# Optimization experiments

Hardware: AMD Instinct MI355X
Metric: run time of the kernel (lower is better)

## Reference

```python
import jax, jax.numpy as jnp
import numpy as np


def setup_inputs() -> dict:
    key = jax.random.key(0)
    ks = jax.random.split(key, 32)
    B, S, H, E, Vs, T = 32, 400, 512, 300, 200, 32
    EN, V = 50000, 50200
    rn = lambda k, shape, s=0.05: jax.random.normal(k, shape, jnp.float32) * s
    return {
        'encoder_hidden': rn(ks[0], (B, S, 2 * H), 1.0),
        'hidden0': rn(ks[1], (B, H), 1.0),
        'user_embed': rn(ks[2], (B, E), 1.0),
        'W_embed': rn(ks[3], (EN, E), 1.0),
        'W_ih': rn(ks[4], (3 * H, E)), 'W_hh': rn(ks[5], (3 * H, H)),
        'b_ih': rn(ks[6], (3 * H,)), 'b_hh': rn(ks[7], (3 * H,)),
        'Wk_c': rn(ks[8], (2 * H, H)), 'bk_c': rn(ks[9], (H,)),
        'Wq_c': rn(ks[10], (H, H)), 'bq_c': rn(ks[11], (H,)),
        'we_c': rn(ks[12], (H,)), 'be_c': rn(ks[13], (1,)),
        'Wk_u': rn(ks[14], (E, H)), 'bk_u': rn(ks[15], (H,)),
        'Wq_u': rn(ks[16], (H, H)), 'bq_u': rn(ks[17], (H,)),
        'we_u': rn(ks[18], (H,)), 'be_u': rn(ks[19], (1,)),
        'Wc': rn(ks[20], (3 * H + 2 * E, H)),
        'Wg': rn(ks[21], (3 * H + E,)), 'bg': rn(ks[22], (1,)),
        'Wgen': rn(ks[23], (H, EN)),
        'src_mask': jnp.ones((B, S), jnp.int32),
        'tgt_': jax.random.randint(ks[24], (B, T), 0, EN),
        'specific_vocab': jax.random.randint(ks[25], (B, Vs), 0, EN),
        'vocab_size': V,
    }


def reference(encoder_hidden, hidden0, user_embed, W_embed, W_ih, W_hh, b_ih, b_hh,
              Wk_c, bk_c, Wq_c, bq_c, we_c, be_c, Wk_u, bk_u, Wq_u, bq_u, we_u, be_u,
              Wc, Wg, bg, Wgen, src_mask, tgt_, specific_vocab, vocab_size):
    B, T = tgt_.shape
    # teacher forcing: prev token embed, step 0 uses <s> token id 1
    tgt_embed = W_embed[tgt_]                                  # [B,T,E]
    init_embed = jnp.broadcast_to(W_embed[1], (B, 1, W_embed.shape[1]))
    prev = jnp.concatenate([init_embed, tgt_embed[:, :T - 1]], axis=1)
    xs = jnp.swapaxes(prev, 0, 1)                              # [T,B,E]

    user_vocab_emb = W_embed[specific_vocab]                   # [B,Vs,E]
    proj_key_c = encoder_hidden @ Wk_c + bk_c                  # [B,S,H]
    proj_key_u = user_vocab_emb @ Wk_u + bk_u                  # [B,Vs,H]
    mask = src_mask != 0
    batch_idx = jnp.arange(B)[:, None]

    def gru_cell(h, x):
        gi = x @ W_ih.T + b_ih
        gh = h @ W_hh.T + b_hh
        i_r, i_z, i_n = jnp.split(gi, 3, axis=-1)
        h_r, h_z, h_n = jnp.split(gh, 3, axis=-1)
        r = jax.nn.sigmoid(i_r + h_r)
        z = jax.nn.sigmoid(i_z + h_z)
        n = jnp.tanh(i_n + r * h_n)
        return (1.0 - z) * n + z * h

    def step(h, x):
        h = gru_cell(h, x)                                     # [B,H]
        q = h
        # Bahdanau attention over encoder states
        sc = jnp.tanh((q @ Wq_c + bq_c)[:, None, :] + proj_key_c) @ we_c + be_c  # [B,S]
        sc = jnp.where(mask, sc, -1e9)
        ac = jax.nn.softmax(sc, axis=-1)
        ctx_c = jnp.einsum('bs,bsd->bd', ac, encoder_hidden)   # [B,2H]
        # Bahdanau attention over user-specific vocab embeddings
        su = jnp.tanh((q @ Wq_u + bq_u)[:, None, :] + proj_key_u) @ we_u + be_u  # [B,Vs]
        au = jax.nn.softmax(su, axis=-1)
        ctx_u = jnp.einsum('bv,bve->be', au, user_vocab_emb)   # [B,E]
        ch = jnp.tanh(jnp.concatenate([q, ctx_c, ctx_u, user_embed], axis=-1) @ Wc)
        gen_prob = jax.nn.softmax(ch @ Wgen, axis=-1)          # [B,embed_num]
        gen_prob = jnp.pad(gen_prob, ((0, 0), (0, vocab_size - gen_prob.shape[-1])))
        copy_prob = jnp.zeros((B, vocab_size), gen_prob.dtype).at[batch_idx, specific_vocab].add(au)
        copy_p = jax.nn.sigmoid(jnp.concatenate([ctx_c, q, ctx_u], axis=-1) @ Wg + bg[0])[:, None]
        mix = copy_p * copy_prob + (1.0 - copy_p) * gen_prob   # [B,vocab]
        return h, mix

    _, probs = jax.lax.scan(step, hidden0, xs)                 # [T,B,V]
    return jnp.swapaxes(probs, 0, 1)                           # [B,T,V]
```

## Files before the change

kernel.cpp:

```cpp
#include <hip/hip_runtime.h>


typedef __attribute__((ext_vector_type(8))) short short8;
typedef __attribute__((ext_vector_type(4))) float f32x4;
typedef unsigned short us;

#define SCW (-2.8853900817779268f)

__device__ __forceinline__ float bf2f(us u) {
  return __uint_as_float(((unsigned)u) << 16);
}
__device__ __forceinline__ us f2bf(float f) {
  unsigned x = __float_as_uint(f);
  unsigned r = x + 0x7fffu + ((x >> 16) & 1u);
  return (us)(r >> 16);
}
__device__ __forceinline__ float fsigmoid(float x) { return 1.f / (1.f + __expf(-x)); }
__device__ __forceinline__ float ftanh(float x) {
  float t = __expf(-2.f * fabsf(x));
  float r = (1.f - t) / (1.f + t);
  return x >= 0.f ? r : -r;
}
__device__ __forceinline__ float ftanh_fast(float x) {
  float u = exp2f(SCW * fabsf(x));
  float r = (1.f - u) * __builtin_amdgcn_rcpf(1.f + u);
  return copysignf(r, x);
}
__device__ __forceinline__ void unpack8(uint4 v, float* f) {
  f[0] = bf2f((us)(v.x & 0xffff)); f[1] = bf2f((us)(v.x >> 16));
  f[2] = bf2f((us)(v.y & 0xffff)); f[3] = bf2f((us)(v.y >> 16));
  f[4] = bf2f((us)(v.z & 0xffff)); f[5] = bf2f((us)(v.z >> 16));
  f[6] = bf2f((us)(v.w & 0xffff)); f[7] = bf2f((us)(v.w >> 16));
}

struct PP {
  const float *enc, *hidden0, *Wk_c, *Wk_u, *Wq_c, *Wq_u, *Wc, *W_ih, *W_hh, *W_embed;
  const int *tgt, *sv;
  us *encb, *hball, *WkcT, *WkuT, *WqcuT, *WcT, *WihT, *WhhF, *xe, *uve;
};

__device__ void tcast_job(const float* __restrict__ src, us* __restrict__ dst,
                          int R, int C, int Rpad, int x, int y, float scale,
                          int lt, float* tb) {
  int tx = lt & 31, ty = lt >> 5;
  int c0 = x * 32, r0 = y * 32;
#pragma unroll
  for (int i = 0; i < 4; ++i) {
    int r = r0 + ty + i * 8, c = c0 + tx;
    tb[(ty + i * 8) * 33 + tx] = (r < R && c < C) ? src[(size_t)r * C + c] : 0.f;
  }
  __syncthreads();
#pragma unroll
  for (int i = 0; i < 4; ++i) {
    int c = c0 + ty + i * 8, rr = r0 + tx;
    if (c < C && rr < Rpad)
      dst[(size_t)c * Rpad + rr] = f2bf(scale * tb[tx * 33 + ty + i * 8]);
  }
}

__global__ __launch_bounds__(256) void k_prep(PP P) {
  __shared__ float tb[32 * 33];
  const int bid = blockIdx.x, tid = threadIdx.x;
  if (bid < 1024) {
    for (int i = bid * 256 + tid; i < 3276800; i += 1024 * 256) {
      float4 v = ((const float4*)P.enc)[i];
      ushort4 o;
      o.x = f2bf(v.x); o.y = f2bf(v.y); o.z = f2bf(v.z); o.w = f2bf(v.w);
      ((ushort4*)P.encb)[i] = o;
    }
  } else if (bid < 1040) {
    int i = (bid - 1024) * 256 + tid;
    float4 v = ((const float4*)P.hidden0)[i];
    ushort4 o;
    o.x = f2bf(v.x); o.y = f2bf(v.y); o.z = f2bf(v.z); o.w = f2bf(v.w);
    ((ushort4*)P.hball)[i] = o;
  } else if (bid < 1552) {
    int j = bid - 1040;
    tcast_job(P.Wk_c, P.WkcT, 1024, 512, 1024, j & 15, j >> 4, SCW, tid, tb);
  } else if (bid < 1712) {
    int j = bid - 1552;
    tcast_job(P.Wk_u, P.WkuT, 300, 512, 320, j % 16, j / 16, SCW, tid, tb);
  } else if (bid < 1968) {
    int j = bid - 1712;
    tcast_job(P.Wq_c, P.WqcuT, 512, 512, 512, j & 15, j >> 4, SCW, tid, tb);
  } else if (bid < 2224) {
    int j = bid - 1968;
    tcast_job(P.Wq_u, P.WqcuT + 512ull * 512, 512, 512, 512, j & 15, j >> 4, SCW, tid, tb);
  } else if (bid < 3296) {
    int j = bid - 2224;
    tcast_job(P.Wc, P.WcT, 2136, 512, 2144, j % 16, j / 16, 1.f, tid, tb);
  } else if (bid < 3680) {
    int row = (bid - 3296) * 4 + (tid >> 6), k = tid & 63;
    for (int kk = k; kk < 320; kk += 64)
      P.WihT[(size_t)row * 320 + kk] =
          (kk < 300) ? f2bf(P.W_ih[(size_t)row * 300 + kk]) : (us)0;
  } else if (bid < 4064) {
    int job = (bid - 3680) * 4 + (tid >> 6), l = tid & 63;
    int q = job / 192, rem = job - q * 192, lt2 = rem >> 4, kt = rem & 15;
    int localrow = lt2 * 16 + (l & 15);
    int g = localrow >> 6, jj = localrow & 63;
    const float* src =
        P.W_hh + (size_t)(g * 512 + q * 64 + jj) * 512 + kt * 32 + (l >> 4) * 8;
    us* dst = P.WhhF + (((size_t)(q * 12 + lt2) * 16 + kt) * 64 + l) * 8;
#pragma unroll
    for (int i = 0; i < 8; ++i) dst[i] = f2bf(src[i]);
  } else if (bid < 4320) {
    int r = (bid - 4064) * 4 + (tid >> 6), k = tid & 63;
    int t = r >> 5, b = r & 31;
    int tok = (t == 0) ? 1 : P.tgt[b * 32 + (t - 1)];
    const float* src = P.W_embed + (size_t)tok * 300;
    for (int kk = k; kk < 320; kk += 64)
      P.xe[(size_t)r * 320 + kk] = (kk < 300) ? f2bf(src[kk]) : (us)0;
  } else {
    int row = (bid - 4320) * 4 + (tid >> 6), k = tid & 63;
    int tok = P.sv[row];
    const float* src = P.W_embed + (size_t)tok * 300;
    for (int kk = k; kk < 320; kk += 64)
      P.uve[(size_t)row * 320 + kk] = (kk < 300) ? f2bf(src[kk]) : (us)0;
  }
}

__global__ __launch_bounds__(256) void k_tcastX(const float* __restrict__ src0,
                                                us* __restrict__ dst0,
                                                int R, int C, int Rpad,
                                                size_t srcB, size_t dstB) {
  __shared__ float tile[32 * 33];
  const float* src = src0 + (size_t)blockIdx.z * srcB;
  us* dst = dst0 + (size_t)blockIdx.z * dstB;
  tcast_job(src, dst, R, C, Rpad, blockIdx.x, blockIdx.y, 1.f, threadIdx.x, tile);
}
__global__ __launch_bounds__(256) void k_tcastXb(const us* __restrict__ src0,
                                                 us* __restrict__ dst0,
                                                 int R, int C, int Rpad,
                                                 size_t srcB, size_t dstB) {
  __shared__ us tile[32][33];
  const us* src = src0 + (size_t)blockIdx.z * srcB;
  us* dst = dst0 + (size_t)blockIdx.z * dstB;
  int c0 = blockIdx.x * 32, r0 = blockIdx.y * 32;
  int tx = threadIdx.x & 31, ty = threadIdx.x >> 5;
#pragma unroll
  for (int i = 0; i < 4; ++i) {
    int r = r0 + ty + i * 8, c = c0 + tx;
    tile[ty + i * 8][tx] = (r < R && c < C) ? src[(size_t)r * C + c] : (us)0;
  }
  __syncthreads();
#pragma unroll
  for (int i = 0; i < 4; ++i) {
    int c = c0 + ty + i * 8, rr = r0 + tx;
    if (c < C && rr < Rpad) dst[(size_t)c * Rpad + rr] = tile[tx][ty + i * 8];
  }
}

template <int MODE, bool NM = false>
__global__ __launch_bounds__(512) void gemm_bt(const us* __restrict__ A,
                                               const us* __restrict__ BT,
                                               int M, int N, int K, int Ntiles,
                                               const float* __restrict__ bias,
                                               float bscale,
                                               us* __restrict__ outB,
                                               float* __restrict__ outF,
                                               float* __restrict__ rowsum) {
  __shared__ us sh[12288];
  __shared__ float rs[256];
  us* As = sh;
  us* Bs = sh + 8192;
  const int tid = threadIdx.x;
  const int lane = tid & 63, wid = tid >> 6;
  const int wr = wid >> 1, wc = wid & 1;
  const int bx = blockIdx.x;
  int mt, nt;
  if (NM) { mt = bx & 3; nt = bx >> 2; }
  else { mt = bx / Ntiles; nt = bx - mt * Ntiles; }
  const int m0 = mt * 256, n0 = nt * 128;
  f32x4 acc[4][4] = {};
  for (int kk = 0; kk < K; kk += 32) {
    uint4 av0, av1, bv;
    {
      int c = tid, row = c >> 2, c8 = (c & 3) * 8;
      av0 = *(const uint4*)(A + (size_t)(m0 + row) * K + kk + c8);
      c = tid + 512; row = c >> 2; c8 = (c & 3) * 8;
      av1 = *(const uint4*)(A + (size_t)(m0 + row) * K + kk + c8);
      c = tid; row = c >> 2; c8 = (c & 3) * 8;
      int nr = n0 + row; if (nr > N - 1) nr = N - 1;
      bv = *(const uint4*)(BT + (size_t)nr * K + kk + c8);
    }
    __syncthreads();
    ((uint4*)As)[tid] = av0;
    ((uint4*)As)[tid + 512] = av1;
    ((uint4*)Bs)[tid] = bv;
    __syncthreads();
    short8 af[4], bfr[4];
#pragma unroll
    for (int m = 0; m < 4; ++m)
      af[m] = *(const short8*)(As + (wr * 64 + m * 16 + (lane & 15)) * 32 + (lane >> 4) * 8);
#pragma unroll
    for (int n = 0; n < 4; ++n)
      bfr[n] = *(const short8*)(Bs + (wc * 64 + n * 16 + (lane & 15)) * 32 + (lane >> 4) * 8);
#pragma unroll
    for (int m = 0; m < 4; ++m)
#pragma unroll
      for (int n = 0; n < 4; ++n)
        acc[m][n] = __builtin_amdgcn_mfma_f32_16x16x32_bf16(af[m], bfr[n], acc[m][n], 0, 0, 0);
  }
  if (MODE == 0) {
#pragma unroll
    for (int m = 0; m < 4; ++m)
#pragma unroll
      for (int n = 0; n < 4; ++n)
#pragma unroll
        for (int reg = 0; reg < 4; ++reg) {
          int r = m0 + wr * 64 + m * 16 + (lane >> 4) * 4 + reg;
          int c = n0 + wc * 64 + n * 16 + (lane & 15);
          outB[(size_t)r * N + c] = f2bf(acc[m][n][reg] + bscale * bias[c]);
        }
  } else {
    if (tid < 256) rs[tid] = 0.f;
    __syncthreads();
#pragma unroll
    for (int m = 0; m < 4; ++m) {
#pragma unroll
      for (int reg = 0; reg < 4; ++reg) {
        int rloc = wr * 64 + m * 16 + (lane >> 4) * 4 + reg;
        float s = 0.f;
#pragma unroll
        for (int n = 0; n < 4; ++n) {
          int c = n0 + wc * 64 + n * 16 + (lane & 15);
          float e = (c < N) ? __expf(acc[m][n][reg]) : 0.f;
          if (c < N) {
            int r = m0 + rloc;
            size_t obase = (size_t)((r & 31) * 32 + (r >> 5)) * 50200;
            outF[obase + c] = e;
          }
          s += e;
        }
        s += __shfl_xor(s, 1, 64); s += __shfl_xor(s, 2, 64);
        s += __shfl_xor(s, 4, 64); s += __shfl_xor(s, 8, 64);
        if ((lane & 15) == 0) atomicAdd(&rs[rloc], s);
      }
    }
    __syncthreads();
    if (tid < 256) atomicAdd(&rowsum[m0 + tid], rs[tid]);
  }
}

__global__ __launch_bounds__(1024, 1) void gemm_v(const us* __restrict__ A,
                                                  const us* __restrict__ BT,
                                                  us* __restrict__ outB,
                                                  float* __restrict__ rowsum) {
  __shared__ us shp[16384];
  __shared__ float rs[256];
  us* As = shp;
  us* Bs = shp + 8192;
  const int tid = threadIdx.x;
  const int lane = tid & 63, wid = tid >> 6;
  const int wr2 = wid >> 2, wc2 = wid & 3;
  const int bx = blockIdx.x;
  const int mt = bx & 3, nt = bx >> 2;
  const int m0 = mt * 256, n0 = nt * 256;
  const int N = 50000;
  const int srow = tid >> 2, sc8 = (tid & 3) * 8;
  int bnr = n0 + srow; if (bnr > N - 1) bnr = N - 1;
  f32x4 acc[4][4] = {};
  for (int kk = 0; kk < 512; kk += 32) {
    uint4 av = *(const uint4*)(A + (size_t)(m0 + srow) * 512 + kk + sc8);
    uint4 bv = *(const uint4*)(BT + (size_t)bnr * 512 + kk + sc8);
    __syncthreads();
    ((uint4*)As)[tid] = av;
    ((uint4*)Bs)[tid] = bv;
    __syncthreads();
    short8 af[4], bfr[4];
#pragma unroll
    for (int m = 0; m < 4; ++m)
      af[m] = *(const short8*)(As + (wr2 * 64 + m * 16 + (lane & 15)) * 32 + (lane >> 4) * 8);
#pragma unroll
    for (int n = 0; n < 4; ++n)
      bfr[n] = *(const short8*)(Bs + (wc2 * 64 + n * 16 + (lane & 15)) * 32 + (lane >> 4) * 8);
#pragma unroll
    for (int m = 0; m < 4; ++m)
#pragma unroll
      for (int n = 0; n < 4; ++n)
        acc[m][n] = __builtin_amdgcn_mfma_f32_16x16x32_bf16(af[m], bfr[n], acc[m][n], 0, 0, 0);
  }
  if (tid < 256) rs[tid] = 0.f;
  __syncthreads();
  for (int g = 0; g < 4; ++g) {
    if (wr2 == g) {
#pragma unroll
      for (int m = 0; m < 4; ++m)
#pragma unroll
        for (int reg = 0; reg < 4; ++reg) {
          int rloc_g = m * 16 + (lane >> 4) * 4 + reg;
          float s = 0.f;
#pragma unroll
          for (int n = 0; n < 4; ++n) {
            int c = n0 + wc2 * 64 + n * 16 + (lane & 15);
            float e = (c < N) ? __expf(acc[m][n][reg]) : 0.f;
            shp[rloc_g * 256 + wc2 * 64 + n * 16 + (lane & 15)] = f2bf(e);
            s += e;
          }
          s += __shfl_xor(s, 1, 64); s += __shfl_xor(s, 2, 64);
          s += __shfl_xor(s, 4, 64); s += __shfl_xor(s, 8, 64);
          if ((lane & 15) == 0) atomicAdd(&rs[g * 64 + rloc_g], s);
        }
    }
    __syncthreads();
#pragma unroll
    for (int k2 = 0; k2 < 2; ++k2) {
      int idx = tid + k2 * 1024;
      int l = idx >> 5, u = idx & 31;
      int r = m0 + g * 64 + l;
      size_t obase = (size_t)((r & 31) * 32 + (r >> 5)) * 50200;
      *(uint4*)(outB + obase + n0 + u * 8) = *(const uint4*)(shp + l * 256 + u * 8);
    }
    __syncthreads();
  }
  if (tid < 256) atomicAdd(&rowsum[m0 + tid], rs[tid]);
}

template <int MODE>
__global__ __launch_bounds__(256) void gemm_med(const us* __restrict__ A,
                                                const us* __restrict__ BT,
                                                int M, int N, int K, int Ntiles,
                                                const float* __restrict__ bias,
                                                float bscale,
                                                us* __restrict__ outB) {
  __shared__ us As[64 * 32];
  __shared__ us Bs[128 * 32];
  const int tid = threadIdx.x, lane = tid & 63, w = tid >> 6;
  const int bx = blockIdx.x;
  const int mt = bx / Ntiles, nt = bx - mt * Ntiles;
  const int m0 = mt * 64, n0 = nt * 128;
  f32x4 acc[4][2] = {};
  for (int kk = 0; kk < K; kk += 32) {
    uint4 av, bv0, bv1;
    av = *(const uint4*)(A + (size_t)(m0 + (tid >> 2)) * K + kk + (tid & 3) * 8);
    {
      int i0 = tid * 2, i1 = tid * 2 + 1;
      bv0 = *(const uint4*)(BT + (size_t)(n0 + (i0 >> 2)) * K + kk + (i0 & 3) * 8);
      bv1 = *(const uint4*)(BT + (size_t)(n0 + (i1 >> 2)) * K + kk + (i1 & 3) * 8);
    }
    __syncthreads();
    ((uint4*)As)[tid] = av;
    ((uint4*)Bs)[tid * 2] = bv0;
    ((uint4*)Bs)[tid * 2 + 1] = bv1;
    __syncthreads();
    short8 af[4], bf0, bf1;
#pragma unroll
    for (int m = 0; m < 4; ++m)
      af[m] = *(const short8*)(As + (m * 16 + (lane & 15)) * 32 + (lane >> 4) * 8);
    bf0 = *(const short8*)(Bs + ((w * 2 + 0) * 16 + (lane & 15)) * 32 + (lane >> 4) * 8);
    bf1 = *(const short8*)(Bs + ((w * 2 + 1) * 16 + (lane & 15)) * 32 + (lane >> 4) * 8);
#pragma unroll
    for (int m = 0; m < 4; ++m) {
      acc[m][0] = __builtin_amdgcn_mfma_f32_16x16x32_bf16(af[m], bf0, acc[m][0], 0, 0, 0);
      acc[m][1] = __builtin_amdgcn_mfma_f32_16x16x32_bf16(af[m], bf1, acc[m][1], 0, 0, 0);
    }
  }
#pragma unroll
  for (int m = 0; m < 4; ++m)
#pragma unroll
    for (int q = 0; q < 2; ++q)
#pragma unroll
      for (int reg = 0; reg < 4; ++reg) {
        int r = m0 + m * 16 + (lane >> 4) * 4 + reg;
        int c = n0 + (w * 2 + q) * 16 + (lane & 15);
        float v = acc[m][q][reg];
        if (MODE == 0) v += bscale * bias[c];
        else v = ftanh_fast(v);
        outB[(size_t)r * N + c] = f2bf(v);
      }
}

struct FP {
  const us* frag; const us* gib; const float* bhh; const float* hidden0;
  us* hball; int* arrive;
  const us* encb; const us* WkcT; const float* bkc; us* pkc;
  const us* uve; const us* WkuT; const float* bku; us* pku;
  const float* Wgen; us* WT;
  const float* enc; us* encTp;
  us* uveTp;
};

__device__ void gru_body(const FP& P, int q, int tid, char* pool) {
  us* hs = (us*)pool;
  float* gh = (float*)(pool + 32768);
  const int lane = tid & 63, w = tid >> 6;
  short8 bfr[16];
  {
    const us* fb = P.frag + (((size_t)(q * 12 + w) * 16) * 64 + lane) * 8;
#pragma unroll
    for (int kt = 0; kt < 16; ++kt) bfr[kt] = *(const short8*)(fb + (size_t)kt * 512);
  }
  float hprev[3], bh0[3], bh1[3], bh2[3];
#pragma unroll
  for (int s = 0; s < 3; ++s) {
    int i = tid + s * 768;
    if (i < 2048) {
      int b = i >> 6, jj = i & 63, j = q * 64 + jj;
      hprev[s] = P.hidden0[b * 512 + j];
      bh0[s] = P.bhh[j]; bh1[s] = P.bhh[512 + j]; bh2[s] = P.bhh[1024 + j];
    }
  }
  const int sw = (lane & 7) << 3;
  for (int t = 0; t < 32; ++t) {
    float gi0[3], gi1[3], gi2[3];
#pragma unroll
    for (int s = 0; s < 3; ++s) {
      int i = tid + s * 768;
      if (i < 2048) {
        int b = i >> 6, jj = i & 63, j = q * 64 + jj;
        size_t gbase = (size_t)(t * 32 + b) * 1536;
        gi0[s] = bf2f(P.gib[gbase + j]);
        gi1[s] = bf2f(P.gib[gbase + 512 + j]);
        gi2[s] = bf2f(P.gib[gbase + 1024 + j]);
      }
    }
    if (t > 0) {
      if (tid == 0) {
        while (__hip_atomic_load(P.arrive + (t - 1), __ATOMIC_ACQUIRE,
                                 __HIP_MEMORY_SCOPE_AGENT) < 8) {
          __builtin_amdgcn_s_sleep(1);
        }
      }
      __syncthreads();
    }
    const us* hp = P.hball + (size_t)t * 16384;
    for (int i = tid; i < 2048; i += 768)
      ((uint4*)hs)[i ^ ((i >> 6) & 7)] = *(const uint4*)(hp + i * 8);
    __syncthreads();
    f32x4 acc0 = {}, acc1 = {};
#pragma unroll
    for (int kt = 0; kt < 16; ++kt) {
      int base0 = ((lane & 15) * 512 + kt * 32 + (lane >> 4) * 8) ^ sw;
      int base1 = (((lane & 15) + 16) * 512 + kt * 32 + (lane >> 4) * 8) ^ sw;
      short8 a0 = *(const short8*)(hs + base0);
      short8 a1 = *(const short8*)(hs + base1);
      acc0 = __builtin_amdgcn_mfma_f32_16x16x32_bf16(a0, bfr[kt], acc0, 0, 0, 0);
      acc1 = __builtin_amdgcn_mfma_f32_16x16x32_bf16(a1, bfr[kt], acc1, 0, 0, 0);
    }
    {
      int col = w * 16 + (lane & 15);
#pragma unroll
      for (int reg = 0; reg < 4; ++reg) {
        gh[col * 33 + ((lane >> 4) * 4 + reg)] = acc0[reg];
        gh[col * 33 + (16 + (lane >> 4) * 4 + reg)] = acc1[reg];
      }
    }
    __syncthreads();
    us* hbn = P.hball + (size_t)(t + 1) * 16384;
#pragma unroll
    for (int s = 0; s < 3; ++s) {
      int i = tid + s * 768;
      if (i < 2048) {
        int b = i >> 6, jj = i & 63, j = q * 64 + jj;
        float g0 = gh[jj * 33 + b] + bh0[s];
        float g1 = gh[(64 + jj) * 33 + b] + bh1[s];
        float g2 = gh[(128 + jj) * 33 + b] + bh2[s];
        float r_ = fsigmoid(gi0[s] + g0);
        float z_ = fsigmoid(gi1[s] + g1);
        float n_ = ftanh(gi2[s] + r_ * g2);
        float hv = (1.f - z_) * n_ + z_ * hprev[s];
        hprev[s] = hv;
        hbn[b * 512 + j] = f2bf(hv);
      }
    }
    __syncthreads();
    if (tid == 0)
      __hip_atomic_fetch_add(P.arrive + t, 1, __ATOMIC_RELEASE,
                             __HIP_MEMORY_SCOPE_AGENT);
  }
}

__device__ void gemm0_body(const us* A, const us* BT, int N, int K,
                           int mt, int nt, const float* bias, float bscale,
                           us* outB, int tid, char* pool) {
  us* As = (us*)pool;
  us* Bs = (us*)(pool + 16384);
  const bool act = tid < 512;
  const int lane = tid & 63, wid = (tid >> 6) & 7;
  const int wr = wid >> 1, wc = wid & 1;
  const int m0 = mt * 256, n0 = nt * 128;
  f32x4 acc[4][4] = {};
  for (int kk = 0; kk < K; kk += 32) {
    uint4 av0 = {0, 0, 0, 0}, av1 = {0, 0, 0, 0}, bv = {0, 0, 0, 0};
    if (act) {
      int c = tid, row = c >> 2, c8 = (c & 3) * 8;
      av0 = *(const uint4*)(A + (size_t)(m0 + row) * K + kk + c8);
      av1 = *(const uint4*)(A + (size_t)(m0 + 128 + row) * K + kk + c8);
      int nr = n0 + row; if (nr > N - 1) nr = N - 1;
      bv = *(const uint4*)(BT + (size_t)nr * K + kk + c8);
    }
    __syncthreads();
    if (act) {
      ((uint4*)As)[tid] = av0;
      ((uint4*)As)[tid + 512] = av1;
      ((uint4*)Bs)[tid] = bv;
    }
    __syncthreads();
    if (act) {
      short8 af[4], bfr[4];
#pragma unroll
      for (int m = 0; m < 4; ++m)
        af[m] = *(const short8*)(As + (wr * 64 + m * 16 + (lane & 15)) * 32 + (lane >> 4) * 8);
#pragma unroll
      for (int n = 0; n < 4; ++n)
        bfr[n] = *(const short8*)(Bs + (wc * 64 + n * 16 + (lane & 15)) * 32 + (lane >> 4) * 8);
#pragma unroll
      for (int m = 0; m < 4; ++m)
#pragma unroll
        for (int n = 0; n < 4; ++n)
          acc[m][n] = __builtin_amdgcn_mfma_f32_16x16x32_bf16(af[m], bfr[n], acc[m][n], 0, 0, 0);
    }
  }
  if (act) {
#pragma unroll
    for (int m = 0; m < 4; ++m)
#pragma unroll
      for (int n = 0; n < 4; ++n)
#pragma unroll
        for (int reg = 0; reg < 4; ++reg) {
          int r = m0 + wr * 64 + m * 16 + (lane >> 4) * 4 + reg;
          int c = n0 + wc * 64 + n * 16 + (lane & 15);
          outB[(size_t)r * N + c] = f2bf(acc[m][n][reg] + bscale * bias[c]);
        }
  }
}

__global__ __launch_bounds__(768, 1) void k_fat(FP P) {
  __shared__ char pool[58368];
  const int bid = blockIdx.x, tid = threadIdx.x;
  if (bid < 8) { gru_body(P, bid, tid, pool); return; }
  if (bid < 208) {
    int j = bid - 8;
    gemm0_body(P.encb, P.WkcT, 512, 1024, j >> 2, j & 3, P.bkc, SCW, P.pkc, tid, pool);
    return;
  }
  if (bid < 308) {
    int j = bid - 208;
    gemm0_body(P.uve, P.WkuT, 512, 320, j >> 2, j & 3, P.bku, SCW, P.pku, tid, pool);
    return;
  }
  const int g = tid >> 8, lt = tid & 255;
  const int tx = lt & 31, ty = lt >> 5;
  float* tb = (float*)(pool + g * 4224);
  if (bid < 830) {
    int base = (bid - 308) * 3 + g;
    for (int it = 0; it < 16; ++it) {
      int sub = base + it * 1566;
      bool valid = sub < 25008;
      int x = valid ? sub % 1563 : 0, y = valid ? sub / 1563 : 0;
      int c0 = x * 32, r0 = y * 32;
      if (valid) {
#pragma unroll
        for (int i = 0; i < 4; ++i) {
          int r = r0 + ty + i * 8, c = c0 + tx;
          tb[(ty + i * 8) * 33 + tx] =
              (c < 50000) ? P.Wgen[(size_t)r * 50000 + c] : 0.f;
        }
      }
      __syncthreads();
      if (valid) {
#pragma unroll
        for (int i = 0; i < 4; ++i) {
          int c = c0 + ty + i * 8;
          if (c < 50000)
            P.WT[(size_t)c * 512 + r0 + tx] = f2bf(tb[tx * 33 + ty + i * 8]);
        }
      }
      __syncthreads();
    }
    return;
  }
  if (bid < 1108) {
    int base = (bid - 830) * 3 + g;
    for (int it = 0; it < 16; ++it) {
      int sub = base + it * 834;
      bool valid = sub < 13312;
      int x = sub & 31, rem = sub >> 5;
      int y = rem % 13, z = rem / 13;
      const float* src = P.enc + (size_t)z * 409600;
      us* dst = P.encTp + (size_t)z * 425984;
      int c0 = x * 32, r0 = y * 32;
      if (valid) {
#pragma unroll
        for (int i = 0; i < 4; ++i) {
          int r = r0 + ty + i * 8, c = c0 + tx;
          tb[(ty + i * 8) * 33 + tx] = (r < 400) ? src[(size_t)r * 1024 + c] : 0.f;
        }
      }
      __syncthreads();
      if (valid) {
#pragma unroll
        for (int i = 0; i < 4; ++i) {
          int c = c0 + ty + i * 8, rr = r0 + tx;
          if (rr < 416) dst[(size_t)c * 416 + rr] = f2bf(tb[tx * 33 + ty + i * 8]);
        }
      }
      __syncthreads();
    }
    return;
  }
  {
    us* tbu = (us*)tb;
    int base = (bid - 1108) * 3 + g;
    for (int it = 0; it < 16; ++it) {
      int sub = base + it * 141;
      bool valid = sub < 2240;
      int x = sub % 10, rem = sub / 10;
      int y = rem % 7, z = rem / 7;
      const us* src = P.uve + (size_t)z * 64000;
      us* dst = P.uveTp + (size_t)z * 71680;
      int c0 = x * 32, r0 = y * 32;
      if (valid) {
#pragma unroll
        for (int i = 0; i < 4; ++i) {
          int r = r0 + ty + i * 8, c = c0 + tx;
          tbu[(ty + i * 8) * 33 + tx] = (r < 200) ? src[(size_t)r * 320 + c] : (us)0;
        }
      }
      __syncthreads();
      if (valid) {
#pragma unroll
        for (int i = 0; i < 4; ++i) {
          int c = c0 + ty + i * 8, rr = r0 + tx;
          if (rr < 224) dst[(size_t)c * 224 + rr] = tbu[tx * 33 + ty + i * 8];
        }
      }
      __syncthreads();
    }
  }
}

__global__ __launch_bounds__(256) void k_scores(const us* __restrict__ Qall,
                                                const us* __restrict__ pkc,
                                                const us* __restrict__ pku,
                                                const float* __restrict__ wec,
                                                const float* __restrict__ bec,
                                                const float* __restrict__ weu,
                                                const float* __restrict__ beu,
                                                const int* __restrict__ src_mask,
                                                float* __restrict__ sc_enc,
                                                float* __restrict__ sc_usr) {
  __shared__ us q[16 * 512];
  const int bid = blockIdx.x;
  const bool enc = bid < 1600;
  int b, s0, th, qoff, S;
  if (enc) {
    b = bid / 50;
    int r = bid % 50;
    s0 = (r >> 1) * 16; th = r & 1; qoff = 0; S = 400;
  } else {
    int j = bid - 1600;
    b = j / 26;
    int r = j % 26;
    s0 = (r >> 1) * 16; th = r & 1; qoff = 512; S = 200;
  }
  for (int i = threadIdx.x; i < 1024; i += 256) {
    int tt = th * 16 + (i >> 6), c8 = (i & 63) * 8;
    ((uint4*)q)[i] = *(const uint4*)(Qall + (size_t)(tt * 32 + b) * 1024 + qoff + c8);
  }
  const int w = threadIdx.x >> 6, lane = threadIdx.x & 63;
  const int d0 = lane * 8;
  const float* we = enc ? wec : weu;
  float wef[8];
  {
    float4 w0 = *(const float4*)(we + d0);
    float4 w1 = *(const float4*)(we + d0 + 4);
    wef[0] = w0.x; wef[1] = w0.y; wef[2] = w0.z; wef[3] = w0.w;
    wef[4] = w1.x; wef[5] = w1.y; wef[6] = w1.z; wef[7] = w1.w;
  }
  const float bias = enc ? bec[0] : beu[0];
  float pkf[4][8];
  int ss[4], validv[4], maskedv[4];
#pragma unroll
  for (int si = 0; si < 4; ++si) {
    int s = s0 + w * 4 + si;
    validv[si] = (s < S);
    int sc = validv[si] ? s : (S - 1);
    ss[si] = sc;
    const us* pk = enc ? pkc + ((size_t)b * 400 + sc) * 512
                       : pku + ((size_t)b * 200 + sc) * 512;
    unpack8(*(const uint4*)(pk + d0), pkf[si]);
    maskedv[si] = enc ? (src_mask[b * 400 + sc] == 0) : 0;
  }
  __syncthreads();
  for (int tl = 0; tl < 16; ++tl) {
    short8 qv = *(const short8*)(q + tl * 512 + d0);
    float qf[8];
#pragma unroll
    for (int d = 0; d < 8; ++d) qf[d] = bf2f((us)qv[d]);
#pragma unroll
    for (int si = 0; si < 4; ++si) {
      float a = 0.f;
#pragma unroll
      for (int d = 0; d < 8; ++d) {
        float x = qf[d] + pkf[si][d];
        float u = exp2f(-fabsf(x));
        float r2v = (1.f - u) * __builtin_amdgcn_rcpf(1.f + u);
        a = fmaf(copysignf(r2v, -x), wef[d], a);
      }
#pragma unroll
      for (int m = 1; m < 64; m <<= 1) a += __shfl_xor(a, m, 64);
      if (lane == 0 && validv[si]) {
        int t = th * 16 + tl;
        float v = a + bias;
        if (enc) sc_enc[(size_t)(t * 32 + b) * 400 + ss[si]] = maskedv[si] ? -1e9f : v;
        else sc_usr[(size_t)(t * 32 + b) * 200 + ss[si]] = v;
      }
    }
  }
}

__device__ __forceinline__ float bmax256(float v, float* r4, int tid) {
#pragma unroll
  for (int m = 1; m < 64; m <<= 1) v = fmaxf(v, __shfl_xor(v, m, 64));
  if ((tid & 63) == 0) r4[tid >> 6] = v;
  __syncthreads();
  float x = fmaxf(fmaxf(r4[0], r4[1]), fmaxf(r4[2], r4[3]));
  __syncthreads();
  return x;
}
__device__ __forceinline__ float bsum256(float v, float* r4, int tid) {
#pragma unroll
  for (int m = 1; m < 64; m <<= 1) v += __shfl_xor(v, m, 64);
  if ((tid & 63) == 0) r4[tid >> 6] = v;
  __syncthreads();
  float x = r4[0] + r4[1] + r4[2] + r4[3];
  __syncthreads();
  return x;
}

__global__ __launch_bounds__(256) void k_soft2(const float* __restrict__ sc_enc,
                                               const float* __restrict__ sc_usr,
                                               us* __restrict__ AC,
                                               us* __restrict__ AU,
                                               float* __restrict__ aual,
                                               float* __restrict__ cp_acc,
                                               const us* __restrict__ hball,
                                               const float* __restrict__ ue,
                                               const float* __restrict__ Wg,
                                               us* __restrict__ catall) {
  __shared__ float r4[4];
  int bid = blockIdx.x, tid = threadIdx.x;
  if (bid < 1024) {
    int t = bid >> 5, b = bid & 31;
    float v0 = (tid < 400) ? sc_enc[(size_t)bid * 400 + tid] : -3e38f;
    float v1 = (tid + 256 < 400) ? sc_enc[(size_t)bid * 400 + tid + 256] : -3e38f;
    float mx = bmax256(fmaxf(v0, v1), r4, tid);
    float e0 = (tid < 400) ? __expf(v0 - mx) : 0.f;
    float e1 = (tid + 256 < 400) ? __expf(v1 - mx) : 0.f;
    float inv = 1.f / bsum256(e0 + e1, r4, tid);
    us* ACb = AC + (size_t)(b * 32 + t) * 416;
    if (tid < 400) ACb[tid] = f2bf(e0 * inv);
    int s2 = tid + 256;
    if (s2 < 400) ACb[s2] = f2bf(e1 * inv);
    else if (s2 < 416) ACb[s2] = 0;
  } else if (bid < 2048) {
    int rr = bid - 1024;
    int t = rr >> 5, b = rr & 31;
    float v0 = (tid < 200) ? sc_usr[(size_t)rr * 200 + tid] : -3e38f;
    float mx = bmax256(v0, r4, tid);
    float e0 = (tid < 200) ? __expf(v0 - mx) : 0.f;
    float inv = 1.f / bsum256(e0, r4, tid);
    us* AUb = AU + (size_t)(b * 32 + t) * 224;
    if (tid < 200) {
      float a = e0 * inv;
      AUb[tid] = f2bf(a);
      aual[(size_t)rr * 200 + tid] = a;
    } else if (tid < 224) {
      AUb[tid] = 0;
    }
  } else if (bid < 2304) {
    int w = tid >> 6, lane = tid & 63;
    int row = (bid - 2048) * 4 + w;
    int t = row >> 5, b = row & 31;
    us* rowp = catall + (size_t)row * 2144;
    const us* hb = hball + (size_t)(t + 1) * 16384 + b * 512;
    *(uint4*)(rowp + lane * 8) = *(const uint4*)(hb + lane * 8);
    for (int i = lane; i < 308; i += 64)
      rowp[1836 + i] = (i < 300) ? f2bf(ue[b * 300 + i]) : (us)0;
  } else {
    int w = tid >> 6, lane = tid & 63, d0 = lane * 8;
#pragma unroll
    for (int k = 0; k < 2; ++k) {
      int row = (bid - 2304) * 8 + w * 2 + k;
      int t = row >> 5, b = row & 31;
      float hv[8];
      unpack8(*(const uint4*)(hball + (size_t)(t + 1) * 16384 + b * 512 + d0), hv);
      float4 g0 = *(const float4*)(Wg + 1024 + d0);
      float4 g1 = *(const float4*)(Wg + 1024 + d0 + 4);
      float a = hv[0] * g0.x + hv[1] * g0.y + hv[2] * g0.z + hv[3] * g0.w +
                hv[4] * g1.x + hv[5] * g1.y + hv[6] * g1.z + hv[7] * g1.w;
#pragma unroll
      for (int m = 1; m < 64; m <<= 1) a += __shfl_xor(a, m, 64);
      if (lane == 0) atomicAdd(&cp_acc[row], a);
    }
  }
}

__device__ void ctx_core(const us* Ab, const us* Bb, const float* Wg,
                         us* catall, float* cp_acc, int b, int N, int Kp,
                         int n0, int catOff, int wgOff, int Nvalid, int tid,
                         us* As, us* Bs, float* gaccs) {
  const int lane = tid & 63, w = tid >> 6;
  if (tid < 32) gaccs[tid] = 0.f;
  f32x4 acc[2][2] = {};
  for (int kk = 0; kk < Kp; kk += 32) {
    uint4 av, bv0, bv1;
    if (tid < 128) av = *(const uint4*)(Ab + (size_t)(tid >> 2) * Kp + kk + (tid & 3) * 8);
    {
      int i0 = tid * 2, row0 = i0 >> 2, c0 = (i0 & 3) * 8;
      int i1 = tid * 2 + 1, row1 = i1 >> 2, c1 = (i1 & 3) * 8;
      int nr0 = n0 + row0; if (nr0 > N - 1) nr0 = N - 1;
      int nr1 = n0 + row1; if (nr1 > N - 1) nr1 = N - 1;
      bv0 = *(const uint4*)(Bb + (size_t)nr0 * Kp + kk + c0);
      bv1 = *(const uint4*)(Bb + (size_t)nr1 * Kp + kk + c1);
    }
    __syncthreads();
    if (tid < 128) ((uint4*)As)[tid] = av;
    ((uint4*)Bs)[tid * 2] = bv0;
    ((uint4*)Bs)[tid * 2 + 1] = bv1;
    __syncthreads();
    short8 a0 = *(const short8*)(As + ((lane & 15)) * 32 + (lane >> 4) * 8);
    short8 a1 = *(const short8*)(As + (16 + (lane & 15)) * 32 + (lane >> 4) * 8);
#pragma unroll
    for (int qq = 0; qq < 2; ++qq) {
      short8 bf_ = *(const short8*)(Bs + ((w * 2 + qq) * 16 + (lane & 15)) * 32 + (lane >> 4) * 8);
      acc[0][qq] = __builtin_amdgcn_mfma_f32_16x16x32_bf16(a0, bf_, acc[0][qq], 0, 0, 0);
      acc[1][qq] = __builtin_amdgcn_mfma_f32_16x16x32_bf16(a1, bf_, acc[1][qq], 0, 0, 0);
    }
  }
#pragma unroll
  for (int mt = 0; mt < 2; ++mt)
#pragma unroll
    for (int qq = 0; qq < 2; ++qq)
#pragma unroll
      for (int reg = 0; reg < 4; ++reg) {
        int t_ = mt * 16 + (lane >> 4) * 4 + reg;
        int c = n0 + (w * 2 + qq) * 16 + (lane & 15);
        if (c < Nvalid) {
          float v = acc[mt][qq][reg];
          catall[(size_t)(t_ * 32 + b) * 2144 + catOff + c] = f2bf(v);
          atomicAdd(&gaccs[t_], v * Wg[wgOff + c]);
        }
      }
  __syncthreads();
  if (tid < 32) atomicAdd(&cp_acc[tid * 32 + b], gaccs[tid]);
}

__global__ __launch_bounds__(256) void k_ctx2(const us* __restrict__ AC,
                                              const us* __restrict__ encTp,
                                              const us* __restrict__ AU,
                                              const us* __restrict__ uveTp,
                                              const float* __restrict__ Wg,
                                              us* __restrict__ catall,
                                              float* __restrict__ cp_acc) {
  __shared__ us As[32 * 32];
  __shared__ us Bs[128 * 32];
  __shared__ float gaccs[32];
  int bid = blockIdx.x, tid = threadIdx.x;
  if (bid < 256) {
    int b = bid >> 3, nt = bid & 7;
    ctx_core(AC + (size_t)b * 32 * 416, encTp + (size_t)b * 1024 * 416, Wg,
             catall, cp_acc, b, 1024, 416, nt * 128, 512, 0, 1024, tid, As, Bs, gaccs);
  } else {
    int j = bid - 256;
    int b = j / 3, nt = j % 3;
    ctx_core(AU + (size_t)b * 32 * 224, uveTp + (size_t)b * 320 * 224, Wg,
             catall, cp_acc, b, 320, 224, nt * 128, 1536, 1536, 300, tid, As, Bs, gaccs);
  }
}

__global__ __launch_bounds__(256) void k_finalize(float* __restrict__ out,
                                                  const float* __restrict__ rowsum,
                                                  const float* __restrict__ cp_acc,
                                                  const float* __restrict__ bg,
                                                  const float* __restrict__ au_all,
                                                  const int* __restrict__ sv) {
  int r = blockIdx.x, t = threadIdx.x;
  int b = r & 31, tt = r >> 5;
  float cp = fsigmoid(cp_acc[r] + bg[0]);
  float scale = (1.f - cp) / rowsum[r];
  float* base = out + (size_t)(b * 32 + tt) * 50200;
  float4* b4 = (float4*)base;
  for (int i = t; i < 12550; i += 256) {
    if (i < 12500) {
      float4 v = b4[i];
      v.x *= scale; v.y *= scale; v.z *= scale; v.w *= scale;
      b4[i] = v;
    } else {
      b4[i] = make_float4(0.f, 0.f, 0.f, 0.f);
    }
  }
  __syncthreads();
  if (t < 200) {
    int idx = sv[b * 200 + t];
    atomicAdd(base + idx, cp * au_all[(size_t)r * 200 + t]);
  }
}

__global__ __launch_bounds__(256) void k_finalize2(const us* __restrict__ expb,
                                                   const float* __restrict__ rowsum,
                                                   const float* __restrict__ cp_acc,
                                                   const float* __restrict__ bg,
                                                   const float* __restrict__ au_all,
                                                   const int* __restrict__ sv,
                                                   float* __restrict__ out) {
  int r = blockIdx.x, t = threadIdx.x;
  int b = r & 31, tt = r >> 5;
  float cp = fsigmoid(cp_acc[r] + bg[0]);
  float scale = (1.f - cp) / rowsum[r];
  size_t obase = (size_t)(b * 32 + tt) * 50200;
  const uint4* eb = (const uint4*)(expb + obase);
  float4* ob = (float4*)(out + obase);
  for (int i = t; i < 6275; i += 256) {
    float4 o0, o1;
    if (i < 6250) {
      uint4 ev = eb[i];
      o0.x = bf2f((us)(ev.x & 0xffff)) * scale; o0.y = bf2f((us)(ev.x >> 16)) * scale;
      o0.z = bf2f((us)(ev.y & 0xffff)) * scale; o0.w = bf2f((us)(ev.y >> 16)) * scale;
      o1.x = bf2f((us)(ev.z & 0xffff)) * scale; o1.y = bf2f((us)(ev.z >> 16)) * scale;
      o1.z = bf2f((us)(ev.w & 0xffff)) * scale; o1.w = bf2f((us)(ev.w >> 16)) * scale;
    } else {
      o0 = make_float4(0.f, 0.f, 0.f, 0.f);
      o1 = o0;
    }
    ob[i * 2] = o0;
    ob[i * 2 + 1] = o1;
  }
  __syncthreads();
  if (t < 200) {
    int idx = sv[b * 200 + t];
    atomicAdd(out + obase + idx, cp * au_all[(size_t)r * 200 + t]);
  }
}


extern "C" void kernel_launch(void* const* d_in, const int* in_sizes, int n_in,
                              void* d_out, int out_size, void* d_ws, size_t ws_size,
                              hipStream_t stream) {
  (void)in_sizes; (void)n_in; (void)out_size;
  const float* enc = (const float*)d_in[0];
  const float* hidden0 = (const float*)d_in[1];
  const float* user_embed = (const float*)d_in[2];
  const float* W_embed = (const float*)d_in[3];
  const float* W_ih = (const float*)d_in[4];
  const float* W_hh = (const float*)d_in[5];
  const float* b_ih = (const float*)d_in[6];
  const float* b_hh = (const float*)d_in[7];
  const float* Wk_c = (const float*)d_in[8];
  const float* bk_c = (const float*)d_in[9];
  const float* Wq_c = (const float*)d_in[10];
  const float* bq_c = (const float*)d_in[11];
  const float* we_c = (const float*)d_in[12];
  const float* be_c = (const float*)d_in[13];
  const float* Wk_u = (const float*)d_in[14];
  const float* bk_u = (const float*)d_in[15];
  const float* Wq_u = (const float*)d_in[16];
  const float* bq_u = (const float*)d_in[17];
  const float* we_u = (const float*)d_in[18];
  const float* be_u = (const float*)d_in[19];
  const float* Wc = (const float*)d_in[20];
  const float* Wg = (const float*)d_in[21];
  const float* bg = (const float*)d_in[22];
  const float* Wgen = (const float*)d_in[23];
  const int* src_mask = (const int*)d_in[24];
  const int* tgt = (const int*)d_in[25];
  const int* sv = (const int*)d_in[26];
  float* out = (float*)d_out;

  char* base = (char*)d_ws;
  size_t off = 0;
  auto take = [&](size_t bytes) {
    char* p = base + off;
    off += (bytes + 255) & ~(size_t)255;
    return p;
  };
  us* WT = (us*)take(50000ull * 512 * 2);
  char* R0 = take(32ull * 1024 * 416 * 2);
  us* encb = (us*)R0;
  char* RCD = take(12800ull * 512 * 2 + 6400ull * 512 * 2);
  us* pkc = (us*)RCD;
  us* pku = (us*)(RCD + 12800ull * 512 * 2);
  us* AC = (us*)RCD;
  us* AU = (us*)(RCD + 860160);
  float* aual = (float*)(RCD + 860160 + 458752);
  us* catall = (us*)(RCD + 860160 + 458752 + 819200);
  us* chb = (us*)(RCD + 860160 + 458752 + 819200 + 4390912);
  us* uve = (us*)take(6400ull * 320 * 2);
  us* uveTp = (us*)take(32ull * 320 * 224 * 2);
  char* RG = take(2700000);
  us* WkcT = (us*)RG;
  us* WihT = (us*)(RG + 1048576);
  us* xe = (us*)(RG + 1048576 + 983040);
  us* WkuT = (us*)take(512ull * 320 * 2);
  us* WqcuT = (us*)take(1024ull * 512 * 2);
  us* WcT = (us*)take(512ull * 2144 * 2);
  us* WhhF = (us*)take(1536ull * 512 * 2);
  us* gib = (us*)take(1024ull * 1536 * 2);
  us* hball = (us*)take(33ull * 16384 * 2);
  us* Qall = (us*)take(1024ull * 1024 * 2);
  float* sc_enc = (float*)take(1024ull * 400 * 4);
  float* sc_usr = (float*)take(1024ull * 200 * 4);
  float* bqcu = (float*)take(1024 * 4);
  float* cp_acc = (float*)take(1024 * 4);
  float* rsum = (float*)take(1024 * 4);
  int* arrive = (int*)take(32 * 4);
  size_t expb_bytes = 1024ull * 50200 * 2;
  bool big_ws = (ws_size >= off + expb_bytes + 256);
  us* expb = big_ws ? (us*)take(expb_bytes) : nullptr;
  us* encTp = big_ws ? expb : (us*)R0;

  hipMemcpyAsync(bqcu, bq_c, 512 * 4, hipMemcpyDeviceToDevice, stream);
  hipMemcpyAsync(bqcu + 512, bq_u, 512 * 4, hipMemcpyDeviceToDevice, stream);
  hipMemsetAsync(rsum, 0, 1024 * 4, stream);
  hipMemsetAsync(cp_acc, 0, 1024 * 4, stream);
  hipMemsetAsync(arrive, 0, 32 * 4, stream);

  PP pp;
  pp.enc = enc; pp.hidden0 = hidden0; pp.Wk_c = Wk_c; pp.Wk_u = Wk_u;
  pp.Wq_c = Wq_c; pp.Wq_u = Wq_u; pp.Wc = Wc; pp.W_ih = W_ih; pp.W_hh = W_hh;
  pp.W_embed = W_embed; pp.tgt = tgt; pp.sv = sv;
  pp.encb = encb; pp.hball = hball; pp.WkcT = WkcT; pp.WkuT = WkuT;
  pp.WqcuT = WqcuT; pp.WcT = WcT; pp.WihT = WihT; pp.WhhF = WhhF;
  pp.xe = xe; pp.uve = uve;
  k_prep<<<5920, 256, 0, stream>>>(pp);
  gemm_med<0><<<192, 256, 0, stream>>>(xe, WihT, 1024, 1536, 320, 12, b_ih, 1.f, gib);

  FP fp;
  fp.frag = WhhF; fp.gib = gib; fp.bhh = b_hh; fp.hidden0 = hidden0;
  fp.hball = hball; fp.arrive = arrive;
  fp.encb = encb; fp.WkcT = WkcT; fp.bkc = bk_c; fp.pkc = pkc;
  fp.uve = uve; fp.WkuT = WkuT; fp.bku = bk_u; fp.pku = pku;
  fp.Wgen = Wgen; fp.WT = WT; fp.enc = enc; fp.encTp = encTp; fp.uveTp = uveTp;

  if (big_ws) {
    k_fat<<<1155, 768, 0, stream>>>(fp);
  } else {
    k_tcastX<<<dim3(1563, 16, 1), 256, 0, stream>>>(Wgen, WT, 512, 50000, 512, 0, 0);
    gemm_bt<0><<<200, 512, 0, stream>>>(encb, WkcT, 12800, 512, 1024, 4, bk_c, SCW,
                                        pkc, nullptr, nullptr);
    gemm_bt<0><<<100, 512, 0, stream>>>(uve, WkuT, 6400, 512, 320, 4, bk_u, SCW,
                                        pku, nullptr, nullptr);
    k_tcastX<<<dim3(32, 13, 32), 256, 0, stream>>>(enc, encTp, 400, 1024, 416,
                                                   400ull * 1024, 1024ull * 416);
    k_tcastXb<<<dim3(10, 7, 32), 256, 0, stream>>>(uve, uveTp, 200, 320, 224,
                                                   200ull * 320, 320ull * 224);
    k_fat<<<8, 768, 0, stream>>>(fp);
  }

  gemm_med<0><<<128, 256, 0, stream>>>(hball + 16384, WqcuT, 1024, 1024, 512, 8,
                                       bqcu, SCW, Qall);
  k_scores<<<2432, 256, 0, stream>>>(Qall, pkc, pku, we_c, be_c, we_u, be_u,
                                     src_mask, sc_enc, sc_usr);
  k_soft2<<<2432, 256, 0, stream>>>(sc_enc, sc_usr, AC, AU, aual, cp_acc,
                                    hball, user_embed, Wg, catall);
  k_ctx2<<<352, 256, 0, stream>>>(AC, encTp, AU, uveTp, Wg, catall, cp_acc);
  gemm_med<2><<<64, 256, 0, stream>>>(catall, WcT, 1024, 512, 2144, 4, nullptr,
                                      1.f, chb);
  if (big_ws) {
    gemm_v<<<784, 1024, 0, stream>>>(chb, WT, expb, rsum);
    k_finalize2<<<1024, 256, 0, stream>>>(expb, rsum, cp_acc, bg, aual, sv, out);
  } else {
    gemm_bt<1, true><<<4 * 391, 512, 0, stream>>>(chb, WT, 1024, 50000, 512, 391,
                                                  nullptr, 1.f, nullptr, out, rsum);
    k_finalize<<<1024, 256, 0, stream>>>(out, rsum, cp_acc, bg, aual, sv);
  }
}
```

Baseline: 705.3 us.

## Retile vocab GEMM to 256x128 blocks with swizzled LDS and per-block flags

The large vocabulary-projection GEMM moves from 1024-thread 256x256 tiles to 512-thread 256x128 tiles with launch bounds allowing several blocks per CU. It uses a K-step of 64, XOR-swizzled shared-memory layouts to reduce bank conflicts, and a per-m-subtile epilogue that stages rows through padded LDS. The goal is better occupancy and latency hiding in the dominant GEMM, at the cost of loading A twice as often per output column. Separately, the GRU step barrier replaces a shared atomic counter with per-block flag stores that each waiter polls, avoiding contention on one atomic.

Result: slower. 841.8 us (+19.4%).

```diff
diff --git a/kernel.cpp b/kernel.cpp
--- a/kernel.cpp
+++ b/kernel.cpp
@@ -243,74 +243,102 @@
   }
 }
 
-__global__ __launch_bounds__(1024, 1) void gemm_v(const us* __restrict__ A,
+__global__ __launch_bounds__(512, 4) void gemm_v2(const us* __restrict__ A,
                                                   const us* __restrict__ BT,
                                                   us* __restrict__ outB,
                                                   float* __restrict__ rowsum) {
-  __shared__ us shp[16384];
+  __shared__ us sh[24576];
   __shared__ float rs[256];
-  us* As = shp;
-  us* Bs = shp + 8192;
+  us* As = sh;
+  us* Bs = sh + 16384;
   const int tid = threadIdx.x;
   const int lane = tid & 63, wid = tid >> 6;
-  const int wr2 = wid >> 2, wc2 = wid & 3;
+  const int wr = wid >> 1, wc = wid & 1;
   const int bx = blockIdx.x;
   const int mt = bx & 3, nt = bx >> 2;
-  const int m0 = mt * 256, n0 = nt * 256;
+  const int m0 = mt * 256, n0 = nt * 128;
   const int N = 50000;
-  const int srow = tid >> 2, sc8 = (tid & 3) * 8;
-  int bnr = n0 + srow; if (bnr > N - 1) bnr = N - 1;
   f32x4 acc[4][4] = {};
-  for (int kk = 0; kk < 512; kk += 32) {
-    uint4 av = *(const uint4*)(A + (size_t)(m0 + srow) * 512 + kk + sc8);
-    uint4 bv = *(const uint4*)(BT + (size_t)bnr * 512 + kk + sc8);
-    __syncthreads();
-    ((uint4*)As)[tid] = av;
-    ((uint4*)Bs)[tid] = bv;
-    __syncthreads();
-    short8 af[4], bfr[4];
-#pragma unroll
-    for (int m = 0; m < 4; ++m)
-      af[m] = *(const short8*)(As + (wr2 * 64 + m * 16 + (lane & 15)) * 32 + (lane >> 4) * 8);
-#pragma unroll
-    for (int n = 0; n < 4; ++n)
-      bfr[n] = *(const short8*)(Bs + (wc2 * 64 + n * 16 + (lane & 15)) * 32 + (lane >> 4) * 8);
-#pragma unroll
-    for (int m = 0; m < 4; ++m)
-#pragma unroll
-      for (int n = 0; n < 4; ++n)
-        acc[m][n] = __builtin_amdgcn_mfma_f32_16x16x32_bf16(af[m], bfr[n], acc[m][n], 0, 0, 0);
+  for (int kk = 0; kk < 512; kk += 64) {
+    uint4 av[4], bv[2];
+#pragma unroll
+    for (int k = 0; k < 4; ++k) {
+      int idx = tid + k * 512;
+      int row = idx >> 3, c8 = (idx & 7) * 8;
+      av[k] = *(const uint4*)(A + (size_t)(m0 + row) * 512 + kk + c8);
+    }
+#pragma unroll
+    for (int k = 0; k < 2; ++k) {
+      int idx = tid + k * 512;
+      int row = idx >> 3, c8 = (idx & 7) * 8;
+      int nr = n0 + row; if (nr > N - 1) nr = N - 1;
+      bv[k] = *(const uint4*)(BT + (size_t)nr * 512 + kk + c8);
+    }
+    __syncthreads();
+#pragma unroll
+    for (int k = 0; k < 4; ++k) {
+      int idx = tid + k * 512;
+      int row = idx >> 3, slot = idx & 7;
+      ((uint4*)As)[(row << 3) | (slot ^ (row & 7))] = av[k];
+    }
+#pragma unroll
+    for (int k = 0; k < 2; ++k) {
+      int idx = tid + k * 512;
+      int row = idx >> 3, slot = idx & 7;
+      ((uint4*)Bs)[(row << 3) | (slot ^ (row & 7))] = bv[k];
+    }
+    __syncthreads();
+#pragma unroll
+    for (int k2 = 0; k2 < 2; ++k2) {
+      short8 af[4], bfr[4];
+#pragma unroll
+      for (int m = 0; m < 4; ++m) {
+        int r2 = wr * 64 + m * 16 + (lane & 15);
+        int slot = k2 * 4 + (lane >> 4);
+        af[m] = *(const short8*)(As + r2 * 64 + ((slot ^ (r2 & 7)) << 3));
+      }
+#pragma unroll
+      for (int n = 0; n < 4; ++n) {
+        int r3 = wc * 64 + n * 16 + (lane & 15);
+        int slot = k2 * 4 + (lane >> 4);
+        bfr[n] = *(const short8*)(Bs + r3 * 64 + ((slot ^ (r3 & 7)) << 3));
+      }
+#pragma unroll
+      for (int m = 0; m < 4; ++m)
+#pragma unroll
+        for (int n = 0; n < 4; ++n)
+          acc[m][n] = __builtin_amdgcn_mfma_f32_16x16x32_bf16(af[m], bfr[n], acc[m][n], 0, 0, 0);
+    }
   }
   if (tid < 256) rs[tid] = 0.f;
   __syncthreads();
-  for (int g = 0; g < 4; ++g) {
-    if (wr2 == g) {
-#pragma unroll
-      for (int m = 0; m < 4; ++m)
-#pragma unroll
-        for (int reg = 0; reg < 4; ++reg) {
-          int rloc_g = m * 16 + (lane >> 4) * 4 + reg;
-          float s = 0.f;
-#pragma unroll
-          for (int n = 0; n < 4; ++n) {
-            int c = n0 + wc2 * 64 + n * 16 + (lane & 15);
-            float e = (c < N) ? __expf(acc[m][n][reg]) : 0.f;
-            shp[rloc_g * 256 + wc2 * 64 + n * 16 + (lane & 15)] = f2bf(e);
-            s += e;
-          }
-          s += __shfl_xor(s, 1, 64); s += __shfl_xor(s, 2, 64);
-          s += __shfl_xor(s, 4, 64); s += __shfl_xor(s, 8, 64);
-          if ((lane & 15) == 0) atomicAdd(&rs[g * 64 + rloc_g], s);
-        }
+#pragma unroll
+  for (int m = 0; m < 4; ++m) {
+#pragma unroll
+    for (int reg = 0; reg < 4; ++reg) {
+      int rloc = wr * 64 + m * 16 + (lane >> 4) * 4 + reg;
+      float s = 0.f;
+#pragma unroll
+      for (int n = 0; n < 4; ++n) {
+        int c = n0 + wc * 64 + n * 16 + (lane & 15);
+        float e = (c < N) ? __expf(acc[m][n][reg]) : 0.f;
+        int lrow = wr * 16 + (lane >> 4) * 4 + reg;
+        int lcol = wc * 64 + n * 16 + (lane & 15);
+        sh[lrow * 136 + lcol] = f2bf(e);
+        s += e;
+      }
+      s += __shfl_xor(s, 1, 64); s += __shfl_xor(s, 2, 64);
+      s += __shfl_xor(s, 4, 64); s += __shfl_xor(s, 8, 64);
+      if ((lane & 15) == 0) atomicAdd(&rs[rloc], s);
     }
     __syncthreads();
 #pragma unroll
     for (int k2 = 0; k2 < 2; ++k2) {
-      int idx = tid + k2 * 1024;
-      int l = idx >> 5, u = idx & 31;
-      int r = m0 + g * 64 + l;
+      int idx = tid + k2 * 512;
+      int l = idx >> 4, u = idx & 15;
+      int r = m0 + (l >> 4) * 64 + m * 16 + (l & 15);
       size_t obase = (size_t)((r & 31) * 32 + (r >> 5)) * 50200;
-      *(uint4*)(outB + obase + n0 + u * 8) = *(const uint4*)(shp + l * 256 + u * 8);
+      *(uint4*)(outB + obase + n0 + u * 8) = *(const uint4*)(sh + l * 136 + u * 8);
     }
     __syncthreads();
   }
@@ -417,9 +445,13 @@
     }
     if (t > 0) {
       if (tid == 0) {
-        while (__hip_atomic_load(P.arrive + (t - 1), __ATOMIC_ACQUIRE,
-                                 __HIP_MEMORY_SCOPE_AGENT) < 8) {
-          __builtin_amdgcn_s_sleep(1);
+        const int* fl = P.arrive + (t - 1) * 8;
+#pragma unroll
+        for (int qq = 0; qq < 8; ++qq) {
+          while (__hip_atomic_load(fl + qq, __ATOMIC_ACQUIRE,
+                                   __HIP_MEMORY_SCOPE_AGENT) == 0) {
+            __builtin_amdgcn_s_sleep(1);
+          }
         }
       }
       __syncthreads();
@@ -466,8 +498,8 @@
     }
     __syncthreads();
     if (tid == 0)
-      __hip_atomic_fetch_add(P.arrive + t, 1, __ATOMIC_RELEASE,
-                             __HIP_MEMORY_SCOPE_AGENT);
+      __hip_atomic_store(P.arrive + t * 8 + q, 1, __ATOMIC_RELEASE,
+                         __HIP_MEMORY_SCOPE_AGENT);
   }
 }
 
@@ -1005,7 +1037,7 @@
   float* bqcu = (float*)take(1024 * 4);
   float* cp_acc = (float*)take(1024 * 4);
   float* rsum = (float*)take(1024 * 4);
-  int* arrive = (int*)take(32 * 4);
+  int* arrive = (int*)take(256 * 4);
   size_t expb_bytes = 1024ull * 50200 * 2;
   bool big_ws = (ws_size >= off + expb_bytes + 256);
   us* expb = big_ws ? (us*)take(expb_bytes) : nullptr;
@@ -1015,7 +1047,7 @@
   hipMemcpyAsync(bqcu + 512, bq_u, 512 * 4, hipMemcpyDeviceToDevice, stream);
   hipMemsetAsync(rsum, 0, 1024 * 4, stream);
   hipMemsetAsync(cp_acc, 0, 1024 * 4, stream);
-  hipMemsetAsync(arrive, 0, 32 * 4, stream);
+  hipMemsetAsync(arrive, 0, 256 * 4, stream);
 
   PP pp;
   pp.enc = enc; pp.hidden0 = hidden0; pp.Wk_c = Wk_c; pp.Wk_u = Wk_u;
@@ -1059,7 +1091,7 @@
   gemm_med<2><<<64, 256, 0, stream>>>(catall, WcT, 1024, 512, 2144, 4, nullptr,
                                       1.f, chb);
   if (big_ws) {
-    gemm_v<<<784, 1024, 0, stream>>>(chb, WT, expb, rsum);
+    gemm_v2<<<1564, 512, 0, stream>>>(chb, WT, expb, rsum);
     k_finalize2<<<1024, 256, 0, stream>>>(expb, rsum, cp_acc, bg, aual, sv, out);
   } else {
     gemm_bt<1, true><<<4 * 391, 512, 0, stream>>>(chb, WT, 1024, 50000, 512, 391,
```
